# Kernel tuning notes

Measured on AMD Instinct MI355X. Metric: run time of the kernel, lower is better.

The kernel has to match this reference:

```python
import jax, jax.numpy as jnp
import numpy as np

B, C, H, W = 8, 80, 128, 128
K = 100
MAX_OBJS = 128
N_GT = 256  # 32 GT boxes per image
HM_W, WH_W, OFF_W = 1.0, 0.1, 1.0
BETA = 0.1  # iou_map weight ('Ct IoU Loss x 0.1')


def setup_inputs() -> dict:
    key = jax.random.key(0)
    ks = jax.random.split(key, 12)
    hm = jax.random.normal(ks[0], (B, C, H, W), jnp.float32)
    wh = jax.random.normal(ks[1], (B, 2, H, W), jnp.float32) * 2.0 + 8.0
    reg = jax.random.normal(ks[2], (B, 2, H, W), jnp.float32) * 0.1
    hm_target = jax.random.uniform(ks[3], (B, C, H, W), jnp.float32) * 0.99
    wh_target = jax.random.uniform(ks[4], (B, MAX_OBJS, 2), jnp.float32) * 20.0 + 2.0
    reg_target = jax.random.uniform(ks[5], (B, MAX_OBJS, 2), jnp.float32)
    reg_mask = jax.random.randint(ks[6], (B, MAX_OBJS), 0, 2).astype(jnp.int32)
    ind = jax.random.randint(ks[7], (B, MAX_OBJS), 0, H * W).astype(jnp.int32)
    cx = jax.random.uniform(ks[8], (N_GT,)) * (W - 1)
    cy = jax.random.uniform(ks[9], (N_GT,)) * (H - 1)
    bw = jax.random.uniform(ks[10], (N_GT,)) * 30.0 + 2.0
    bh = jax.random.uniform(ks[11], (N_GT,)) * 30.0 + 2.0
    target_box = jnp.stack([cx - bw / 2, cy - bh / 2, cx + bw / 2, cy + bh / 2], -1).astype(jnp.float32)
    target_bidx = jnp.repeat(jnp.arange(B), N_GT // B).astype(jnp.int32)
    return {"hm": hm, "wh": wh, "reg": reg, "hm_target": hm_target,
            "wh_target": wh_target, "reg_target": reg_target,
            "reg_mask": reg_mask, "ind": ind,
            "target_box": target_box, "target_bidx": target_bidx}


def _gather_feat(feat, ind):
    # feat [B, ch, H, W], ind [B, M] spatial indices -> [B, M, ch]
    b, ch = feat.shape[0], feat.shape[1]
    f = feat.reshape(b, ch, -1).transpose(0, 2, 1)  # [B, HW, ch]
    return jnp.take_along_axis(f, ind[:, :, None], axis=1)


def _pairwise_iou(boxes1, boxes2):
    # boxes1 [K,4], boxes2 [N,4], xyxy -> [K,N]
    a1 = jnp.maximum(boxes1[:, 2] - boxes1[:, 0], 0.0) * jnp.maximum(boxes1[:, 3] - boxes1[:, 1], 0.0)
    a2 = jnp.maximum(boxes2[:, 2] - boxes2[:, 0], 0.0) * jnp.maximum(boxes2[:, 3] - boxes2[:, 1], 0.0)
    lt = jnp.maximum(boxes1[:, None, :2], boxes2[None, :, :2])
    rb = jnp.minimum(boxes1[:, None, 2:], boxes2[None, :, 2:])
    whi = jnp.clip(rb - lt, 0.0)
    inter = whi[..., 0] * whi[..., 1]
    union = a1[:, None] + a2[None, :] - inter
    return inter / jnp.maximum(union, 1e-7)


def _decode(hm_s, wh, reg):
    # _nms: 3x3 max-pool peak keeping
    hmax = jax.lax.reduce_window(hm_s, -jnp.inf, jax.lax.max,
                                 (1, 1, 3, 3), (1, 1, 1, 1),
                                 [(0, 0), (0, 0), (1, 1), (1, 1)])
    hm_k = jnp.where(hmax == hm_s, hm_s, 0.0)
    # global top-K over C*H*W (equivalent to per-class topK then topK-of-topK)
    scores, inds = jax.lax.top_k(hm_k.reshape(B, -1), K)
    clses = inds // (H * W)
    sinds = inds % (H * W)
    ys_i = sinds // W
    xs_i = sinds % W
    r = _gather_feat(reg, sinds)  # [B,K,2] sub-pixel offsets
    xs = xs_i.astype(jnp.float32) + r[..., 0]
    ys = ys_i.astype(jnp.float32) + r[..., 1]
    w = _gather_feat(wh, sinds)   # [B,K,2]
    boxes = jnp.stack([xs - w[..., 0] / 2, ys - w[..., 1] / 2,
                       xs + w[..., 0] / 2, ys + w[..., 1] / 2], -1)
    return boxes, scores, clses, ys_i, xs_i


def _focal_loss(pred, gt):
    # CenterNet focal loss; pred already sigmoid+clamped
    pos = gt == 1.0
    neg_w = (1.0 - gt) ** 4
    pos_loss = jnp.sum(jnp.where(pos, jnp.log(pred) * (1.0 - pred) ** 2, 0.0))
    neg_loss = jnp.sum(jnp.where(pos, 0.0, jnp.log(1.0 - pred) * pred ** 2 * neg_w))
    num_pos = jnp.sum(pos.astype(jnp.float32))
    return jnp.where(num_pos > 0, -(pos_loss + neg_loss) / jnp.maximum(num_pos, 1.0), -neg_loss)


def _reg_l1(out, mask, ind, tgt):
    pred = _gather_feat(out, ind)                       # [B, M, 2]
    m = jnp.broadcast_to(mask.astype(jnp.float32)[:, :, None], pred.shape)
    return jnp.sum(jnp.abs(pred * m - tgt * m)) / (jnp.sum(m) + 1e-4)


def reference(hm, wh, reg, hm_target, wh_target, reg_target, reg_mask, ind, target_box, target_bidx):
    hm_s = jnp.clip(jax.nn.sigmoid(hm), 1e-4, 1.0 - 1e-4)  # _sigmoid
    boxes, scores, clses, ys_i, xs_i = _decode(hm_s, wh, reg)
    # per-image pairwise IoU vs GT boxes of the same image, max over GT
    iou_all = jax.vmap(lambda bx: _pairwise_iou(bx, target_box))(boxes)  # [B,K,N]
    bmask = target_bidx[None, None, :] == jnp.arange(B)[:, None, None]
    iou = jnp.max(jnp.where(bmask, iou_all, 0.0), axis=-1)              # [B,K]
    # scatter IoU into dense heatmap-shaped iou_map at (b, cls, y, x)
    b_idx = jnp.broadcast_to(jnp.arange(B)[:, None], (B, K))
    iou_map = jnp.zeros_like(hm_s).at[b_idx, clses, ys_i, xs_i].set(iou)
    hm_t = jnp.clip(hm_target + BETA * iou_map, 0.0, 1.0)
    hm_loss = _focal_loss(hm_s, hm_t)
    wh_loss = _reg_l1(wh, reg_mask, ind, wh_target)
    off_loss = _reg_l1(reg, reg_mask, ind, reg_target)
    loss = HM_W * hm_loss + WH_W * wh_loss + OFF_W * off_loss
    return loss, hm_loss, wh_loss, off_loss
```

## Files before the change

### kernel.cpp

```cpp
#include <hip/hip_runtime.h>
#include <math.h>

#define B_ 8
#define C_ 80
#define H_ 128
#define W_ 128
#define K_ 100
#define MAXOBJS_ 128
#define NGT_ 256
#define HW_ (H_*W_)
#define CHW_ (C_*H_*W_)
#define TOT_ (B_*CHW_)
#define NBINS_ 4096
#define BCAP_ 4096
#define DCAP_ 128
#define CAPLDS_ 1536
#define DLOC_ 128
#define BLOC_ 768
#define NEGINF_ (-INFINITY)

#define OFF_LISTCNT 96
#define OFF_HIST   128
#define OFF_THR    131200
#define OFF_CNTA   131264
#define OFF_CNTB   131296
#define OFF_DEFV   131328
#define OFF_DEFI   135424
#define OFF_BORV   139520
#define OFF_BORI   270592
#define OFF_LIST   401664
#define ZERO_BYTES 131328
#define CAP_REQ    196608ull
#define CAP_MAX    262144ull

__device__ __forceinline__ unsigned skey(float x){
    unsigned u = __float_as_uint(x);
    return (u & 0x80000000u) ? ~u : (u | 0x80000000u);
}

__device__ __forceinline__ void find_thr(const unsigned* __restrict__ lh,
                                         unsigned* __restrict__ part,
                                         unsigned target,
                                         unsigned* out_thr, unsigned* out_cum){
    int t = threadIdx.x;
    unsigned s = 0;
    #pragma unroll
    for(int k=0;k<16;++k) s += lh[t*16+k];
    part[t] = s;
    __syncthreads();
    for(int off=1; off<256; off<<=1){
        unsigned v = (t+off<256) ? part[t+off] : 0u;
        __syncthreads();
        part[t] += v;
        __syncthreads();
    }
    unsigned nxt = (t<255) ? part[t+1] : 0u;
    if(part[t] >= target && nxt < target){
        unsigned cum = nxt;
        int thr = t*16;
        for(int bin=t*16+15; bin>=t*16; --bin){
            unsigned c = lh[bin];
            if(cum + c >= target){ thr = bin; break; }
            cum += c;
        }
        *out_thr = (unsigned)thr;
        *out_cum = cum;
    }
    __syncthreads();
}

struct Row { float v[4]; float le, re; };

__device__ __forceinline__ Row loadrow(const float* __restrict__ P, int y, int xq){
    Row r;
    if(y < 0 || y >= H_){
        r.v[0]=r.v[1]=r.v[2]=r.v[3]=r.le=r.re=NEGINF_;
        return r;
    }
    const float4 f = *(const float4*)(P + y*W_ + xq*4);
    r.v[0]=f.x; r.v[1]=f.y; r.v[2]=f.z; r.v[3]=f.w;
    r.le = (xq==0) ? NEGINF_ : P[y*W_ + xq*4 - 1];
    r.re = (xq==31)? NEGINF_ : P[y*W_ + xq*4 + 4];
    return r;
}

__device__ __forceinline__ void hmax4(const Row& r, float h[4]){
    h[0]=fmaxf(fmaxf(r.le,  r.v[0]), r.v[1]);
    h[1]=fmaxf(fmaxf(r.v[0],r.v[1]), r.v[2]);
    h[2]=fmaxf(fmaxf(r.v[1],r.v[2]), r.v[3]);
    h[3]=fmaxf(fmaxf(r.v[2],r.v[3]), r.re);
}

__global__ __launch_bounds__(256) void k_main(const float* __restrict__ hm,
        const float* __restrict__ hmt, unsigned* __restrict__ hist,
        double* __restrict__ accum, unsigned* __restrict__ listcnt,
        int2* __restrict__ list, int capB){
    __shared__ unsigned lh[NBINS_];
    __shared__ int2 lbuf[CAPLDS_];
    __shared__ unsigned lcnt, lbase;
    __shared__ float red[256];
    int t = threadIdx.x;
    int plane = blockIdx.x >> 1;
    int half  = blockIdx.x & 1;
    int b = plane / C_;
    int cls = plane - b*C_;
    const float* P = hm  + (size_t)plane*HW_;
    const float* T = hmt + (size_t)plane*HW_;
    int idx0 = cls*HW_;
    unsigned lane = (unsigned)(t & 63);

    for(int i=t;i<NBINS_;i+=256) lh[i]=0u;
    if(t==0) lcnt=0u;
    __syncthreads();

    int xq = t & 31;
    int y0 = half*64 + (t >> 5) * 8;
    Row rp = loadrow(P, y0-1, xq);
    Row rc = loadrow(P, y0,   xq);
    float hp[4], hc[4];
    hmax4(rp, hp); hmax4(rc, hc);
    float acc = 0.f;
    for(int rr=0; rr<8; ++rr){
        int y = y0 + rr;
        Row rn = loadrow(P, y+1, xq);
        float hn[4]; hmax4(rn, hn);
        float lr[4];
        lr[0]=fmaxf(rc.le,  rc.v[1]);
        lr[1]=fmaxf(rc.v[0],rc.v[2]);
        lr[2]=fmaxf(rc.v[1],rc.v[3]);
        lr[3]=fmaxf(rc.v[2],rc.re);
        float4 tg = *(const float4*)(T + y*W_ + xq*4);
        float tgv[4] = {tg.x, tg.y, tg.z, tg.w};
        #pragma unroll
        for(int j=0;j<4;++j){
            float v = rc.v[j];
            bool pk = (v>=lr[j]) && (v>=hp[j]) && (v>=hn[j]);
            if(pk) atomicAdd(&lh[skey(v)>>20], 1u);
            if(capB){
                unsigned long long mask = __ballot(pk);
                int cnt = __popcll(mask);
                unsigned pre = (unsigned)__popcll(mask & ((1ull<<lane)-1ull));
                int base = 0;
                if(cnt){
                    if(lane==0) base = (int)atomicAdd(&lcnt, (unsigned)cnt);
                    base = __shfl(base, 0, 64);
                }
                if(pk){
                    unsigned p = (unsigned)base + pre;
                    int2 e; e.x = __float_as_int(v); e.y = idx0 + y*W_ + xq*4 + j;
                    if(p < CAPLDS_) lbuf[p] = e;
                    else {
                        unsigned g = atomicAdd(&listcnt[b], 1u);
                        if(g < (unsigned)capB) list[(size_t)b*capB + g] = e;
                    }
                }
            }
            float pr = 1.f/(1.f + __expf(-v));
            pr = fminf(fmaxf(pr, 1e-4f), 1.f - 1e-4f);
            float q = 1.f - tgv[j]; float q2 = q*q;
            acc += __logf(1.f - pr) * pr * pr * q2 * q2;
        }
        rc = rn;
        #pragma unroll
        for(int j=0;j<4;++j){ hp[j]=hc[j]; hc[j]=hn[j]; }
    }
    __syncthreads();
    unsigned n = lcnt; if(n > CAPLDS_) n = CAPLDS_;
    if(capB && t==0) lbase = atomicAdd(&listcnt[b], n);
    for(int i=t;i<NBINS_;i+=256){ unsigned c=lh[i]; if(c) atomicAdd(&hist[b*NBINS_+i], c); }
    red[t] = acc;
    __syncthreads();
    if(capB){
        for(unsigned i=t;i<n;i+=256){
            unsigned g = lbase + i;
            if(g < (unsigned)capB) list[(size_t)b*capB + g] = lbuf[i];
        }
    }
    for(int s=128;s>0;s>>=1){
        if(t<s) red[t]+=red[t+s];
        __syncthreads();
    }
    if(t==0) atomicAdd(&accum[0], (double)red[0]);
}

__global__ void k_thresh(const unsigned* __restrict__ hist, unsigned* __restrict__ thrbin){
    __shared__ unsigned lh[NBINS_];
    __shared__ unsigned part[256];
    __shared__ unsigned thrs, cums;
    int b = blockIdx.x, t = threadIdx.x;
    for(int i=t;i<NBINS_;i+=256) lh[i]=hist[b*NBINS_+i];
    if(t==0){ thrs=0u; cums=0u; }
    __syncthreads();
    find_thr(lh, part, (unsigned)K_, &thrs, &cums);
    if(t==0) thrbin[b]=thrs;
}

__global__ __launch_bounds__(256) void k_scan(const int2* __restrict__ list,
        const unsigned* __restrict__ listcnt, int capB,
        const unsigned* __restrict__ thrbin,
        unsigned* __restrict__ cntA, unsigned* __restrict__ cntB,
        float* __restrict__ defv, int* __restrict__ defi,
        float* __restrict__ borv, int* __restrict__ bori){
    __shared__ int2 dloc[DLOC_];
    __shared__ int2 bloc[BLOC_];
    __shared__ unsigned dc, bc, dbase, bbase;
    int b = blockIdx.x >> 6;
    int chunk = blockIdx.x & 63;
    int t = threadIdx.x;
    if(t==0){ dc=0u; bc=0u; }
    __syncthreads();
    unsigned thr = thrbin[b];
    unsigned n = listcnt[b]; if(n > (unsigned)capB) n = (unsigned)capB;
    for(unsigned i = chunk*256u + t; i < n; i += 64u*256u){
        int2 e = list[(size_t)b*capB + i];
        float v = __int_as_float(e.x);
        unsigned bin = skey(v) >> 20;
        if(bin > thr){
            unsigned p = atomicAdd(&dc, 1u);
            if(p < DLOC_) dloc[p] = e;
            else { unsigned g = atomicAdd(&cntA[b],1u); if(g<DCAP_){ defv[b*DCAP_+g]=v; defi[b*DCAP_+g]=e.y; } }
        } else if(bin == thr){
            unsigned p = atomicAdd(&bc, 1u);
            if(p < BLOC_) bloc[p] = e;
            else { unsigned g = atomicAdd(&cntB[b],1u); if(g<BCAP_){ borv[b*BCAP_+g]=v; bori[b*BCAP_+g]=e.y; } }
        }
    }
    __syncthreads();
    unsigned dn = dc < DLOC_ ? dc : DLOC_;
    unsigned bn = bc < BLOC_ ? bc : BLOC_;
    if(t==0){
        dbase = dn ? atomicAdd(&cntA[b], dn) : 0u;
        bbase = bn ? atomicAdd(&cntB[b], bn) : 0u;
    }
    __syncthreads();
    for(unsigned i=t;i<dn;i+=256){
        unsigned g = dbase + i;
        if(g < DCAP_){ defv[b*DCAP_+g]=__int_as_float(dloc[i].x); defi[b*DCAP_+g]=dloc[i].y; }
    }
    for(unsigned i=t;i<bn;i+=256){
        unsigned g = bbase + i;
        if(g < BCAP_){ borv[b*BCAP_+g]=__int_as_float(bloc[i].x); bori[b*BCAP_+g]=bloc[i].y; }
    }
}

__device__ __forceinline__ bool is_peak_scalar(const float* __restrict__ hm, int idx, float v){
    int w = idx & (W_-1);
    int h = (idx >> 7) & (H_-1);
    bool peak = true;
    #pragma unroll
    for(int dy=-1; dy<=1; ++dy){
        int hh = h + dy;
        if(hh < 0 || hh >= H_) continue;
        #pragma unroll
        for(int dx=-1; dx<=1; ++dx){
            if(dy==0 && dx==0) continue;
            int ww = w + dx;
            if(ww < 0 || ww >= W_) continue;
            peak = peak && (v >= __ldg(&hm[idx + dy*W_ + dx]));
        }
    }
    return peak;
}

__global__ __launch_bounds__(256) void k_collect(const float* __restrict__ hm,
        const unsigned* __restrict__ thrbin,
        unsigned* __restrict__ cntA, unsigned* __restrict__ cntB,
        float* __restrict__ defv, int* __restrict__ defi,
        float* __restrict__ borv, int* __restrict__ bori){
    int idx = blockIdx.x*256 + threadIdx.x;
    float v = hm[idx];
    if(!is_peak_scalar(hm, idx, v)) return;
    int b = idx / CHW_;
    unsigned bin = skey(v) >> 20;
    unsigned thr = thrbin[b];
    if(bin > thr){
        unsigned p = atomicAdd(&cntA[b], 1u);
        if(p < DCAP_){ defv[b*DCAP_+p] = v; defi[b*DCAP_+p] = idx - b*CHW_; }
    } else if(bin == thr){
        unsigned p = atomicAdd(&cntB[b], 1u);
        if(p < BCAP_){ borv[b*BCAP_+p] = v; bori[b*BCAP_+p] = idx - b*CHW_; }
    }
}

__global__ __launch_bounds__(256) void k_select(const float* __restrict__ hm,
        const float* __restrict__ hmt, const float* __restrict__ wh,
        const float* __restrict__ reg, const float* __restrict__ tbox,
        const int* __restrict__ tbid,
        const unsigned* __restrict__ cntA, const unsigned* __restrict__ cntB,
        const float* __restrict__ defv, const int* __restrict__ defi,
        const float* __restrict__ borv, const int* __restrict__ bori,
        double* __restrict__ accum, int* __restrict__ misc){
    int b = blockIdx.x, t = threadIdx.x;
    __shared__ float sbox[NGT_][4];
    __shared__ int   sbid[NGT_];
    __shared__ float sv[BCAP_];
    __shared__ int   si[BCAP_];
    __shared__ unsigned h2[NBINS_];
    __shared__ unsigned t4[BCAP_];
    __shared__ unsigned part[256];
    __shared__ int  rvI[256];
    __shared__ int  sel[K_];
    __shared__ unsigned selc, t3c, t4c;
    __shared__ unsigned thr2s, cum2s, thr3s, need3s;
    __shared__ int wsel;

    int nA = (int)cntA[b]; if(nA>DCAP_) nA=DCAP_; if(nA>K_) nA=K_;
    int nB = (int)cntB[b]; if(nB>BCAP_) nB=BCAP_;
    int m = K_ - nA; if(m>nB) m=nB; if(m<0) m=0;

    for(int i=t;i<NGT_;i+=256){
        sbox[i][0]=tbox[i*4+0]; sbox[i][1]=tbox[i*4+1];
        sbox[i][2]=tbox[i*4+2]; sbox[i][3]=tbox[i*4+3];
        sbid[i]=tbid[i];
    }
    for(int i=t;i<nB;i+=256){ sv[i]=borv[b*BCAP_+i]; si[i]=bori[b*BCAP_+i]; }
    for(int i=t;i<nA;i+=256) sel[i]=defi[b*DCAP_+i];
    if(t==0){ selc=(unsigned)nA; t3c=0u; t4c=0u; thr2s=0u; cum2s=0u; thr3s=0u; need3s=0u; }
    for(int i=t;i<NBINS_;i+=256) h2[i]=0u;
    __syncthreads();

    if(m>0){
        for(int i=t;i<nB;i+=256) atomicAdd(&h2[(skey(sv[i])>>8)&0xFFFu], 1u);
        __syncthreads();
        find_thr(h2, part, (unsigned)m, &thr2s, &cum2s);
        unsigned thr2 = thr2s, need2 = (unsigned)m - cum2s;
        for(int i=t;i<nB;i+=256){
            unsigned sb=(skey(sv[i])>>8)&0xFFFu;
            if(sb>thr2){ unsigned p=atomicAdd(&selc,1u); if(p<K_) sel[p]=si[i]; }
            else if(sb==thr2){ unsigned p=atomicAdd(&t3c,1u); if(p<BCAP_) t4[p]=(unsigned)i; }
        }
        __syncthreads();
        unsigned nt3=t3c; if(nt3>BCAP_) nt3=BCAP_;
        part[t]=0u;
        __syncthreads();
        for(unsigned i=t;i<nt3;i+=256) atomicAdd(&part[skey(sv[t4[i]])&0xFFu], 1u);
        __syncthreads();
        for(int off=1; off<256; off<<=1){
            unsigned v = (t+off<256)? part[t+off] : 0u;
            __syncthreads();
            part[t] += v;
            __syncthreads();
        }
        {
            unsigned nxt = (t<255)? part[t+1] : 0u;
            if(part[t] >= need2 && nxt < need2){ thr3s=(unsigned)t; need3s=need2-nxt; }
        }
        __syncthreads();
        unsigned thr3=thr3s, need3=need3s;
        for(unsigned i=t;i<nt3;i+=256){
            unsigned ci=t4[i];
            unsigned lb=skey(sv[ci])&0xFFu;
            if(lb>thr3){ unsigned p=atomicAdd(&selc,1u); if(p<K_) sel[p]=si[ci]; }
            else if(lb==thr3){ unsigned p=atomicAdd(&t4c,1u); if(p<NBINS_) h2[p]=(unsigned)si[ci]; }
        }
        __syncthreads();
        unsigned n4=t4c; if(n4>NBINS_) n4=NBINS_;
        if(need3 >= n4){
            for(unsigned i=t;i<n4;i+=256){ unsigned p=atomicAdd(&selc,1u); if(p<K_) sel[p]=(int)h2[i]; }
            __syncthreads();
        } else {
            for(unsigned it=0; it<need3; ++it){
                int bi=0x7FFFFFFF;
                for(unsigned i=t;i<n4;i+=256){ int w=(int)h2[i]; bi = (w<bi)?w:bi; }
                rvI[t]=bi;
                __syncthreads();
                for(int st=128;st>0;st>>=1){
                    if(t<st){ int w=rvI[t+st]; if(w<rvI[t]) rvI[t]=w; }
                    __syncthreads();
                }
                if(t==0){ wsel=rvI[0]; unsigned p=selc; selc=p+1u; if(p<K_) sel[p]=wsel; }
                __syncthreads();
                int w=wsel;
                for(unsigned i=t;i<n4;i+=256) if((int)h2[i]==w) h2[i]=0x7FFFFFFFu;
                __syncthreads();
            }
        }
    }
    __syncthreads();

    int nsel=(int)selc; if(nsel>K_) nsel=K_;
    for(int k=t;k<nsel;k+=256){
        int idx = sel[k];
        int cls = idx / HW_;
        int sp  = idx - cls*HW_;
        int yi  = sp >> 7;
        int xi  = sp & (W_-1);
        float r0 = reg[(b*2+0)*HW_ + sp];
        float r1 = reg[(b*2+1)*HW_ + sp];
        float w0 = wh[(b*2+0)*HW_ + sp];
        float w1 = wh[(b*2+1)*HW_ + sp];
        float xs = (float)xi + r0;
        float ys = (float)yi + r1;
        float x1 = xs - w0*0.5f, y1 = ys - w1*0.5f;
        float x2 = xs + w0*0.5f, y2 = ys + w1*0.5f;
        float a1 = fmaxf(x2-x1, 0.f) * fmaxf(y2-y1, 0.f);
        float best = 0.f;
        for(int g=0; g<NGT_; ++g){
            if(sbid[g] != b) continue;
            float gx1=sbox[g][0], gy1=sbox[g][1], gx2=sbox[g][2], gy2=sbox[g][3];
            float a2 = fmaxf(gx2-gx1, 0.f) * fmaxf(gy2-gy1, 0.f);
            float ix1 = fmaxf(x1,gx1), iy1 = fmaxf(y1,gy1);
            float ix2 = fminf(x2,gx2), iy2 = fminf(y2,gy2);
            float iw = fmaxf(ix2-ix1, 0.f), ih = fmaxf(iy2-iy1, 0.f);
            float inter = iw*ih;
            float uni = a1 + a2 - inter;
            float iou = inter / fmaxf(uni, 1e-7f);
            best = fmaxf(best, iou);
        }
        int gidx = b*CHW_ + idx;
        float v = hm[gidx];
        float p = 1.f/(1.f + __expf(-v));
        p = fminf(fmaxf(p, 1e-4f), 1.f - 1e-4f);
        float gt0 = hmt[gidx];
        float q0 = 1.f - gt0; float q02 = q0*q0;
        float neg0 = __logf(1.f - p) * p * p * q02 * q02;
        float gt1 = fminf(gt0 + 0.1f*best, 1.f);
        if(gt1 == 1.f){
            atomicAdd(&misc[0], 1);
            float op = 1.f - p;
            atomicAdd(&accum[1], (double)(__logf(p)*op*op));
            atomicAdd(&accum[2], (double)(-neg0));
        } else {
            float q1 = 1.f - gt1; float q12 = q1*q1;
            float neg1 = __logf(1.f - p) * p * p * q12 * q12;
            atomicAdd(&accum[2], (double)(neg1 - neg0));
        }
    }
}

__global__ void k_regfinal(const float* __restrict__ wh, const float* __restrict__ reg,
        const float* __restrict__ wht, const float* __restrict__ regt,
        const int* __restrict__ mask, const int* __restrict__ ind,
        const double* __restrict__ accum, const int* __restrict__ misc,
        float* __restrict__ out){
    int tid = threadIdx.x;
    float whn = 0.f, offn = 0.f, ms = 0.f;
    for(int i=tid; i<B_*MAXOBJS_; i+=256){
        int b = i / MAXOBJS_;
        float mk = (float)mask[i];
        int id = ind[i];
        float p0 = wh[(b*2+0)*HW_ + id], p1 = wh[(b*2+1)*HW_ + id];
        whn += mk*(fabsf(p0 - wht[2*i]) + fabsf(p1 - wht[2*i+1]));
        float q0 = reg[(b*2+0)*HW_ + id], q1 = reg[(b*2+1)*HW_ + id];
        offn += mk*(fabsf(q0 - regt[2*i]) + fabsf(q1 - regt[2*i+1]));
        ms += 2.f*mk;
    }
    __shared__ float r0[256], r1[256], r2[256];
    r0[tid]=whn; r1[tid]=offn; r2[tid]=ms;
    __syncthreads();
    for(int st=128; st>0; st>>=1){
        if(tid<st){ r0[tid]+=r0[tid+st]; r1[tid]+=r1[tid+st]; r2[tid]+=r2[tid+st]; }
        __syncthreads();
    }
    if(tid==0){
        double neg = accum[0] + accum[2];
        double pos = accum[1];
        int np = misc[0];
        float hm_loss;
        if(np > 0) hm_loss = (float)(-(pos + neg) / (double)(np < 1 ? 1 : np));
        else       hm_loss = (float)(-neg);
        float msum = r2[0];
        float wh_loss  = r0[0] / (msum + 1e-4f);
        float off_loss = r1[0] / (msum + 1e-4f);
        float loss = hm_loss + 0.1f*wh_loss + off_loss;
        out[0]=loss; out[1]=hm_loss; out[2]=wh_loss; out[3]=off_loss;
    }
}

extern "C" void kernel_launch(void* const* d_in, const int* in_sizes, int n_in,
                              void* d_out, int out_size, void* d_ws, size_t ws_size,
                              hipStream_t stream){
    const float* hm   = (const float*)d_in[0];
    const float* wh   = (const float*)d_in[1];
    const float* reg  = (const float*)d_in[2];
    const float* hmt  = (const float*)d_in[3];
    const float* wht  = (const float*)d_in[4];
    const float* regt = (const float*)d_in[5];
    const int*   mask = (const int*)d_in[6];
    const int*   ind  = (const int*)d_in[7];
    const float* tbox = (const float*)d_in[8];
    const int*   tbid = (const int*)d_in[9];

    char* ws = (char*)d_ws;
    double*   accum   = (double*)ws;
    int*      misc    = (int*)(ws + 64);
    unsigned* listcnt = (unsigned*)(ws + OFF_LISTCNT);
    unsigned* hist    = (unsigned*)(ws + OFF_HIST);
    unsigned* thrbin  = (unsigned*)(ws + OFF_THR);
    unsigned* cntA    = (unsigned*)(ws + OFF_CNTA);
    unsigned* cntB    = (unsigned*)(ws + OFF_CNTB);
    float*    defv    = (float*)(ws + OFF_DEFV);
    int*      defi    = (int*)(ws + OFF_DEFI);
    float*    borv    = (float*)(ws + OFF_BORV);
    int*      bori    = (int*)(ws + OFF_BORI);
    int2*     list    = (int2*)(ws + OFF_LIST);

    size_t capB = 0;
    if(ws_size >= (size_t)OFF_LIST + CAP_REQ*(size_t)B_*8ull){
        capB = (ws_size - (size_t)OFF_LIST) / ((size_t)B_*8ull);
        if(capB > CAP_MAX) capB = CAP_MAX;
    }

    hipMemsetAsync(ws, 0, ZERO_BYTES, stream);
    k_main<<<B_*C_*2, 256, 0, stream>>>(hm, hmt, hist, accum, listcnt, list, (int)capB);
    k_thresh<<<B_, 256, 0, stream>>>(hist, thrbin);
    if(capB){
        k_scan<<<B_*64, 256, 0, stream>>>(list, listcnt, (int)capB, thrbin,
                                          cntA, cntB, defv, defi, borv, bori);
    } else {
        k_collect<<<TOT_/256, 256, 0, stream>>>(hm, thrbin, cntA, cntB,
                                                defv, defi, borv, bori);
    }
    k_select<<<B_, 256, 0, stream>>>(hm, hmt, wh, reg, tbox, tbid, cntA, cntB,
                                     defv, defi, borv, bori, accum, misc);
    k_regfinal<<<1, 256, 0, stream>>>(wh, reg, wht, regt, mask, ind, accum, misc,
                                      (float*)d_out);
    (void)in_sizes; (void)n_in; (void)out_size;
}
```

Measured before the change: 98.93 us.

## Fuse threshold and final reduction into preceding kernels via last-block counters

```diff
diff --git a/kernel.cpp b/kernel.cpp
--- a/kernel.cpp
+++ b/kernel.cpp
@@ -14,24 +14,27 @@
 #define NBINS_ 4096
 #define BCAP_ 4096
 #define DCAP_ 128
-#define CAPLDS_ 1536
+#define CAPLDS_ 1024
 #define DLOC_ 128
 #define BLOC_ 768
 #define NEGINF_ (-INFINITY)
 
+#define OFF_MISC    64
 #define OFF_LISTCNT 96
-#define OFF_HIST   128
-#define OFF_THR    131200
-#define OFF_CNTA   131264
-#define OFF_CNTB   131296
-#define OFF_DEFV   131328
-#define OFF_DEFI   135424
-#define OFF_BORV   139520
-#define OFF_BORI   270592
-#define OFF_LIST   401664
-#define ZERO_BYTES 131328
-#define CAP_REQ    196608ull
-#define CAP_MAX    262144ull
+#define OFF_BDONE   128
+#define OFF_SELDONE 160
+#define OFF_THRB    192
+#define OFF_CNTA    224
+#define OFF_CNTB    256
+#define OFF_HIST    512
+#define ZERO_BYTES  131584
+#define OFF_DEFV    131584
+#define OFF_DEFI    135680
+#define OFF_BORV    139776
+#define OFF_BORI    270848
+#define OFF_LIST    401920
+#define CAP_REQ     196608ull
+#define CAP_MAX     262144ull
 
 __device__ __forceinline__ unsigned skey(float x){
     unsigned u = __float_as_uint(x);
@@ -69,36 +72,69 @@
     __syncthreads();
 }
 
-struct Row { float v[4]; float le, re; };
-
-__device__ __forceinline__ Row loadrow(const float* __restrict__ P, int y, int xq){
-    Row r;
-    if(y < 0 || y >= H_){
-        r.v[0]=r.v[1]=r.v[2]=r.v[3]=r.le=r.re=NEGINF_;
-        return r;
-    }
-    const float4 f = *(const float4*)(P + y*W_ + xq*4);
-    r.v[0]=f.x; r.v[1]=f.y; r.v[2]=f.z; r.v[3]=f.w;
-    r.le = (xq==0) ? NEGINF_ : P[y*W_ + xq*4 - 1];
-    r.re = (xq==31)? NEGINF_ : P[y*W_ + xq*4 + 4];
-    return r;
-}
-
-__device__ __forceinline__ void hmax4(const Row& r, float h[4]){
-    h[0]=fmaxf(fmaxf(r.le,  r.v[0]), r.v[1]);
-    h[1]=fmaxf(fmaxf(r.v[0],r.v[1]), r.v[2]);
-    h[2]=fmaxf(fmaxf(r.v[1],r.v[2]), r.v[3]);
-    h[3]=fmaxf(fmaxf(r.v[2],r.v[3]), r.re);
+__device__ __forceinline__ void find_thr_g(const unsigned* __restrict__ gh,
+                                           unsigned* __restrict__ part,
+                                           unsigned target,
+                                           unsigned* out_thr, unsigned* out_cum){
+    int t = threadIdx.x;
+    unsigned loc[16]; unsigned s = 0;
+    #pragma unroll
+    for(int k=0;k<16;++k){
+        loc[k] = __hip_atomic_load(&gh[t*16+k], __ATOMIC_RELAXED, __HIP_MEMORY_SCOPE_AGENT);
+        s += loc[k];
+    }
+    part[t] = s;
+    __syncthreads();
+    for(int off=1; off<256; off<<=1){
+        unsigned v = (t+off<256) ? part[t+off] : 0u;
+        __syncthreads();
+        part[t] += v;
+        __syncthreads();
+    }
+    unsigned nxt = (t<255) ? part[t+1] : 0u;
+    if(part[t] >= target && nxt < target){
+        unsigned cum = nxt; int thr = t*16; bool fnd = false;
+        #pragma unroll
+        for(int k=15;k>=0;--k){
+            if(!fnd){
+                if(cum + loc[k] >= target){ thr = t*16+k; fnd = true; }
+                else cum += loc[k];
+            }
+        }
+        *out_thr = (unsigned)thr;
+        *out_cum = cum;
+    }
+    __syncthreads();
+}
+
+__device__ __forceinline__ void loadrow(const float* __restrict__ P, int y, int xq,
+                                        float4& f, float& le, float& re){
+    if(y >= 0 && y < H_) f = *(const float4*)(P + y*W_ + xq*4);
+    else { f.x = NEGINF_; f.y = NEGINF_; f.z = NEGINF_; f.w = NEGINF_; }
+    float l = __shfl_up(f.w, 1, 32);
+    float r = __shfl_down(f.x, 1, 32);
+    le = (xq==0)  ? NEGINF_ : l;
+    re = (xq==31) ? NEGINF_ : r;
+}
+
+__device__ __forceinline__ void hmax4v(const float4& f, float le, float re, float h[4]){
+    h[0]=fmaxf(fmaxf(le,  f.x), f.y);
+    h[1]=fmaxf(fmaxf(f.x, f.y), f.z);
+    h[2]=fmaxf(fmaxf(f.y, f.z), f.w);
+    h[3]=fmaxf(fmaxf(f.z, f.w), re);
 }
 
 __global__ __launch_bounds__(256) void k_main(const float* __restrict__ hm,
         const float* __restrict__ hmt, unsigned* __restrict__ hist,
         double* __restrict__ accum, unsigned* __restrict__ listcnt,
-        int2* __restrict__ list, int capB){
-    __shared__ unsigned lh[NBINS_];
+        int2* __restrict__ list, int capB, unsigned* __restrict__ bdone,
+        unsigned* __restrict__ thrbin){
+    __shared__ unsigned lhp[NBINS_/2];
     __shared__ int2 lbuf[CAPLDS_];
-    __shared__ unsigned lcnt, lbase;
-    __shared__ float red[256];
+    __shared__ unsigned part[256];
+    __shared__ float wsum[4];
+    __shared__ unsigned lcnt, lbase, thrs, cums;
+    __shared__ int amlast;
     int t = threadIdx.x;
     int plane = blockIdx.x >> 1;
     int half  = blockIdx.x & 1;
@@ -107,46 +143,43 @@
     const float* P = hm  + (size_t)plane*HW_;
     const float* T = hmt + (size_t)plane*HW_;
     int idx0 = cls*HW_;
-    unsigned lane = (unsigned)(t & 63);
-
-    for(int i=t;i<NBINS_;i+=256) lh[i]=0u;
-    if(t==0) lcnt=0u;
+
+    for(int i=t;i<NBINS_/2;i+=256) lhp[i]=0u;
+    if(t==0){ lcnt=0u; thrs=0u; cums=0u; }
     __syncthreads();
 
     int xq = t & 31;
-    int y0 = half*64 + (t >> 5) * 8;
-    Row rp = loadrow(P, y0-1, xq);
-    Row rc = loadrow(P, y0,   xq);
-    float hp[4], hc[4];
-    hmax4(rp, hp); hmax4(rc, hc);
+    int y0 = half*64 + (t>>5)*8;
+
+    float4 vp; float lep, rep;
+    loadrow(P, y0-1, xq, vp, lep, rep);
+    float hp[4]; hmax4v(vp, lep, rep, hp);
+    float4 vc; float lec, rec;
+    loadrow(P, y0, xq, vc, lec, rec);
+
     float acc = 0.f;
     for(int rr=0; rr<8; ++rr){
         int y = y0 + rr;
-        Row rn = loadrow(P, y+1, xq);
-        float hn[4]; hmax4(rn, hn);
-        float lr[4];
-        lr[0]=fmaxf(rc.le,  rc.v[1]);
-        lr[1]=fmaxf(rc.v[0],rc.v[2]);
-        lr[2]=fmaxf(rc.v[1],rc.v[3]);
-        lr[3]=fmaxf(rc.v[2],rc.re);
+        float4 vn; float len, ren;
+        loadrow(P, y+1, xq, vn, len, ren);
+        float hn[4]; hmax4v(vn, len, ren, hn);
+        float vv[4]  = {vc.x, vc.y, vc.z, vc.w};
+        float lrv[4];
+        lrv[0]=fmaxf(lec,  vc.y);
+        lrv[1]=fmaxf(vc.x, vc.z);
+        lrv[2]=fmaxf(vc.y, vc.w);
+        lrv[3]=fmaxf(vc.z, rec);
         float4 tg = *(const float4*)(T + y*W_ + xq*4);
         float tgv[4] = {tg.x, tg.y, tg.z, tg.w};
         #pragma unroll
         for(int j=0;j<4;++j){
-            float v = rc.v[j];
-            bool pk = (v>=lr[j]) && (v>=hp[j]) && (v>=hn[j]);
-            if(pk) atomicAdd(&lh[skey(v)>>20], 1u);
-            if(capB){
-                unsigned long long mask = __ballot(pk);
-                int cnt = __popcll(mask);
-                unsigned pre = (unsigned)__popcll(mask & ((1ull<<lane)-1ull));
-                int base = 0;
-                if(cnt){
-                    if(lane==0) base = (int)atomicAdd(&lcnt, (unsigned)cnt);
-                    base = __shfl(base, 0, 64);
-                }
-                if(pk){
-                    unsigned p = (unsigned)base + pre;
+            float v = vv[j];
+            bool pk = (v>=lrv[j]) && (v>=hp[j]) && (v>=hn[j]);
+            if(pk){
+                unsigned bin = skey(v)>>20;
+                atomicAdd(&lhp[bin>>1], 1u<<((bin&1)<<4));
+                if(capB){
+                    unsigned p = atomicAdd(&lcnt, 1u);
                     int2 e; e.x = __float_as_int(v); e.y = idx0 + y*W_ + xq*4 + j;
                     if(p < CAPLDS_) lbuf[p] = e;
                     else {
@@ -160,15 +193,25 @@
             float q = 1.f - tgv[j]; float q2 = q*q;
             acc += __logf(1.f - pr) * pr * pr * q2 * q2;
         }
-        rc = rn;
         #pragma unroll
-        for(int j=0;j<4;++j){ hp[j]=hc[j]; hc[j]=hn[j]; }
-    }
-    __syncthreads();
+        for(int j=0;j<4;++j) hp[j] = fmaxf(lrv[j], vv[j]);
+        vc = vn; lec = len; rec = ren;
+    }
+    __syncthreads();
+
     unsigned n = lcnt; if(n > CAPLDS_) n = CAPLDS_;
     if(capB && t==0) lbase = atomicAdd(&listcnt[b], n);
-    for(int i=t;i<NBINS_;i+=256){ unsigned c=lh[i]; if(c) atomicAdd(&hist[b*NBINS_+i], c); }
-    red[t] = acc;
+    for(int i=t;i<NBINS_/2;i+=256){
+        unsigned w = lhp[i];
+        if(w){
+            unsigned c0 = w & 0xFFFFu, c1 = w >> 16;
+            if(c0) atomicAdd(&hist[b*NBINS_ + 2*i],     c0);
+            if(c1) atomicAdd(&hist[b*NBINS_ + 2*i + 1], c1);
+        }
+    }
+    #pragma unroll
+    for(int off=32; off>0; off>>=1) acc += __shfl_xor(acc, off, 64);
+    if((t & 63) == 0) wsum[t>>6] = acc;
     __syncthreads();
     if(capB){
         for(unsigned i=t;i<n;i+=256){
@@ -176,23 +219,20 @@
             if(g < (unsigned)capB) list[(size_t)b*capB + g] = lbuf[i];
         }
     }
-    for(int s=128;s>0;s>>=1){
-        if(t<s) red[t]+=red[t+s];
-        __syncthreads();
-    }
-    if(t==0) atomicAdd(&accum[0], (double)red[0]);
-}
-
-__global__ void k_thresh(const unsigned* __restrict__ hist, unsigned* __restrict__ thrbin){
-    __shared__ unsigned lh[NBINS_];
-    __shared__ unsigned part[256];
-    __shared__ unsigned thrs, cums;
-    int b = blockIdx.x, t = threadIdx.x;
-    for(int i=t;i<NBINS_;i+=256) lh[i]=hist[b*NBINS_+i];
-    if(t==0){ thrs=0u; cums=0u; }
-    __syncthreads();
-    find_thr(lh, part, (unsigned)K_, &thrs, &cums);
-    if(t==0) thrbin[b]=thrs;
+    if(t==0) atomicAdd(&accum[0], (double)(wsum[0]+wsum[1]+wsum[2]+wsum[3]));
+
+    __threadfence();
+    __syncthreads();
+    if(t==0){
+        unsigned d = atomicAdd(&bdone[b], 1u);
+        amlast = (d == (unsigned)(2*C_ - 1));
+    }
+    __syncthreads();
+    if(amlast){
+        __threadfence();
+        find_thr_g(&hist[b*NBINS_], part, (unsigned)K_, &thrs, &cums);
+        if(t==0) thrbin[b] = thrs;
+    }
 }
 
 __global__ __launch_bounds__(256) void k_scan(const int2* __restrict__ list,
@@ -286,13 +326,16 @@
         const float* __restrict__ hmt, const float* __restrict__ wh,
         const float* __restrict__ reg, const float* __restrict__ tbox,
         const int* __restrict__ tbid,
+        const float* __restrict__ wht, const float* __restrict__ regt,
+        const int* __restrict__ mask, const int* __restrict__ ind,
         const unsigned* __restrict__ cntA, const unsigned* __restrict__ cntB,
         const float* __restrict__ defv, const int* __restrict__ defi,
         const float* __restrict__ borv, const int* __restrict__ bori,
-        double* __restrict__ accum, int* __restrict__ misc){
+        double* __restrict__ accum, int* __restrict__ misc,
+        unsigned* __restrict__ seldone, float* __restrict__ out){
     int b = blockIdx.x, t = threadIdx.x;
-    __shared__ float sbox[NGT_][4];
-    __shared__ int   sbid[NGT_];
+    __shared__ float gbox[NGT_][4];
+    __shared__ float garea[NGT_];
     __shared__ float sv[BCAP_];
     __shared__ int   si[BCAP_];
     __shared__ unsigned h2[NBINS_];
@@ -300,23 +343,33 @@
     __shared__ unsigned part[256];
     __shared__ int  rvI[256];
     __shared__ int  sel[K_];
-    __shared__ unsigned selc, t3c, t4c;
+    __shared__ float sbx[K_][4];
+    __shared__ float sa[K_];
+    __shared__ int   ioui[K_];
+    __shared__ float r0s[256], r1s[256], r2s[256];
+    __shared__ unsigned gcnt, selc, t3c, t4c;
     __shared__ unsigned thr2s, cum2s, thr3s, need3s;
-    __shared__ int wsel;
+    __shared__ int wsel, amlast;
 
     int nA = (int)cntA[b]; if(nA>DCAP_) nA=DCAP_; if(nA>K_) nA=K_;
     int nB = (int)cntB[b]; if(nB>BCAP_) nB=BCAP_;
     int m = K_ - nA; if(m>nB) m=nB; if(m<0) m=0;
 
+    if(t==0){ gcnt=0u; selc=(unsigned)nA; t3c=0u; t4c=0u;
+              thr2s=0u; cum2s=0u; thr3s=0u; need3s=0u; }
+    for(int i=t;i<NBINS_;i+=256) h2[i]=0u;
+    __syncthreads();
+
     for(int i=t;i<NGT_;i+=256){
-        sbox[i][0]=tbox[i*4+0]; sbox[i][1]=tbox[i*4+1];
-        sbox[i][2]=tbox[i*4+2]; sbox[i][3]=tbox[i*4+3];
-        sbid[i]=tbid[i];
+        if(tbid[i]==b){
+            unsigned p = atomicAdd(&gcnt, 1u);
+            float gx1=tbox[i*4+0], gy1=tbox[i*4+1], gx2=tbox[i*4+2], gy2=tbox[i*4+3];
+            gbox[p][0]=gx1; gbox[p][1]=gy1; gbox[p][2]=gx2; gbox[p][3]=gy2;
+            garea[p]=fmaxf(gx2-gx1,0.f)*fmaxf(gy2-gy1,0.f);
+        }
     }
     for(int i=t;i<nB;i+=256){ sv[i]=borv[b*BCAP_+i]; si[i]=bori[b*BCAP_+i]; }
     for(int i=t;i<nA;i+=256) sel[i]=defi[b*DCAP_+i];
-    if(t==0){ selc=(unsigned)nA; t3c=0u; t4c=0u; thr2s=0u; cum2s=0u; thr3s=0u; need3s=0u; }
-    for(int i=t;i<NBINS_;i+=256) h2[i]=0u;
     __syncthreads();
 
     if(m>0){
@@ -383,31 +436,32 @@
         int idx = sel[k];
         int cls = idx / HW_;
         int sp  = idx - cls*HW_;
-        int yi  = sp >> 7;
-        int xi  = sp & (W_-1);
-        float r0 = reg[(b*2+0)*HW_ + sp];
-        float r1 = reg[(b*2+1)*HW_ + sp];
-        float w0 = wh[(b*2+0)*HW_ + sp];
-        float w1 = wh[(b*2+1)*HW_ + sp];
-        float xs = (float)xi + r0;
-        float ys = (float)yi + r1;
-        float x1 = xs - w0*0.5f, y1 = ys - w1*0.5f;
-        float x2 = xs + w0*0.5f, y2 = ys + w1*0.5f;
-        float a1 = fmaxf(x2-x1, 0.f) * fmaxf(y2-y1, 0.f);
-        float best = 0.f;
-        for(int g=0; g<NGT_; ++g){
-            if(sbid[g] != b) continue;
-            float gx1=sbox[g][0], gy1=sbox[g][1], gx2=sbox[g][2], gy2=sbox[g][3];
-            float a2 = fmaxf(gx2-gx1, 0.f) * fmaxf(gy2-gy1, 0.f);
-            float ix1 = fmaxf(x1,gx1), iy1 = fmaxf(y1,gy1);
-            float ix2 = fminf(x2,gx2), iy2 = fminf(y2,gy2);
-            float iw = fmaxf(ix2-ix1, 0.f), ih = fmaxf(iy2-iy1, 0.f);
-            float inter = iw*ih;
-            float uni = a1 + a2 - inter;
-            float iou = inter / fmaxf(uni, 1e-7f);
-            best = fmaxf(best, iou);
-        }
-        int gidx = b*CHW_ + idx;
+        int yi = sp>>7, xi = sp&(W_-1);
+        float rr0 = reg[(b*2+0)*HW_+sp], rr1 = reg[(b*2+1)*HW_+sp];
+        float w0 = wh[(b*2+0)*HW_+sp],  w1 = wh[(b*2+1)*HW_+sp];
+        float xs = (float)xi + rr0, ys = (float)yi + rr1;
+        float x1=xs-w0*0.5f, y1=ys-w1*0.5f, x2=xs+w0*0.5f, y2=ys+w1*0.5f;
+        sbx[k][0]=x1; sbx[k][1]=y1; sbx[k][2]=x2; sbx[k][3]=y2;
+        sa[k] = fmaxf(x2-x1,0.f)*fmaxf(y2-y1,0.f);
+        ioui[k] = 0;
+    }
+    __syncthreads();
+    int ng = (int)gcnt; if(ng>NGT_) ng=NGT_;
+    for(int pi=t; pi<nsel*ng; pi+=256){
+        int k = pi / ng, g = pi - k*ng;
+        float x1=sbx[k][0], y1=sbx[k][1], x2=sbx[k][2], y2=sbx[k][3];
+        float ix1=fmaxf(x1,gbox[g][0]), iy1=fmaxf(y1,gbox[g][1]);
+        float ix2=fminf(x2,gbox[g][2]), iy2=fminf(y2,gbox[g][3]);
+        float iw=fmaxf(ix2-ix1,0.f), ih=fmaxf(iy2-iy1,0.f);
+        float inter=iw*ih;
+        float uni = sa[k] + garea[g] - inter;
+        float iou = inter / fmaxf(uni, 1e-7f);
+        atomicMax(&ioui[k], __float_as_int(iou));
+    }
+    __syncthreads();
+    for(int k=t;k<nsel;k+=256){
+        float best = __int_as_float(ioui[k]);
+        int gidx = b*CHW_ + sel[k];
         float v = hm[gidx];
         float p = 1.f/(1.f + __expf(-v));
         p = fminf(fmaxf(p, 1e-4f), 1.f - 1e-4f);
@@ -426,44 +480,46 @@
             atomicAdd(&accum[2], (double)(neg1 - neg0));
         }
     }
-}
-
-__global__ void k_regfinal(const float* __restrict__ wh, const float* __restrict__ reg,
-        const float* __restrict__ wht, const float* __restrict__ regt,
-        const int* __restrict__ mask, const int* __restrict__ ind,
-        const double* __restrict__ accum, const int* __restrict__ misc,
-        float* __restrict__ out){
-    int tid = threadIdx.x;
-    float whn = 0.f, offn = 0.f, ms = 0.f;
-    for(int i=tid; i<B_*MAXOBJS_; i+=256){
-        int b = i / MAXOBJS_;
-        float mk = (float)mask[i];
-        int id = ind[i];
-        float p0 = wh[(b*2+0)*HW_ + id], p1 = wh[(b*2+1)*HW_ + id];
-        whn += mk*(fabsf(p0 - wht[2*i]) + fabsf(p1 - wht[2*i+1]));
-        float q0 = reg[(b*2+0)*HW_ + id], q1 = reg[(b*2+1)*HW_ + id];
-        offn += mk*(fabsf(q0 - regt[2*i]) + fabsf(q1 - regt[2*i+1]));
-        ms += 2.f*mk;
-    }
-    __shared__ float r0[256], r1[256], r2[256];
-    r0[tid]=whn; r1[tid]=offn; r2[tid]=ms;
-    __syncthreads();
-    for(int st=128; st>0; st>>=1){
-        if(tid<st){ r0[tid]+=r0[tid+st]; r1[tid]+=r1[tid+st]; r2[tid]+=r2[tid+st]; }
-        __syncthreads();
-    }
-    if(tid==0){
-        double neg = accum[0] + accum[2];
-        double pos = accum[1];
-        int np = misc[0];
-        float hm_loss;
-        if(np > 0) hm_loss = (float)(-(pos + neg) / (double)(np < 1 ? 1 : np));
-        else       hm_loss = (float)(-neg);
-        float msum = r2[0];
-        float wh_loss  = r0[0] / (msum + 1e-4f);
-        float off_loss = r1[0] / (msum + 1e-4f);
-        float loss = hm_loss + 0.1f*wh_loss + off_loss;
-        out[0]=loss; out[1]=hm_loss; out[2]=wh_loss; out[3]=off_loss;
+
+    __threadfence();
+    __syncthreads();
+    if(t==0){
+        unsigned d = atomicAdd(seldone, 1u);
+        amlast = (d == (unsigned)(B_-1));
+    }
+    __syncthreads();
+    if(amlast){
+        __threadfence();
+        float whn=0.f, offn=0.f, ms=0.f;
+        for(int i=t;i<B_*MAXOBJS_;i+=256){
+            int bb = i >> 7;
+            float mk = (float)mask[i];
+            int id = ind[i];
+            float p0 = wh[(bb*2+0)*HW_+id], p1 = wh[(bb*2+1)*HW_+id];
+            whn += mk*(fabsf(p0 - wht[2*i]) + fabsf(p1 - wht[2*i+1]));
+            float q0 = reg[(bb*2+0)*HW_+id], q1 = reg[(bb*2+1)*HW_+id];
+            offn += mk*(fabsf(q0 - regt[2*i]) + fabsf(q1 - regt[2*i+1]));
+            ms += 2.f*mk;
+        }
+        r0s[t]=whn; r1s[t]=offn; r2s[t]=ms;
+        __syncthreads();
+        for(int st=128; st>0; st>>=1){
+            if(t<st){ r0s[t]+=r0s[t+st]; r1s[t]+=r1s[t+st]; r2s[t]+=r2s[t+st]; }
+            __syncthreads();
+        }
+        if(t==0){
+            double nb  = __hip_atomic_load(&accum[0], __ATOMIC_RELAXED, __HIP_MEMORY_SCOPE_AGENT);
+            double pos = __hip_atomic_load(&accum[1], __ATOMIC_RELAXED, __HIP_MEMORY_SCOPE_AGENT);
+            double nd  = __hip_atomic_load(&accum[2], __ATOMIC_RELAXED, __HIP_MEMORY_SCOPE_AGENT);
+            int np = __hip_atomic_load(&misc[0], __ATOMIC_RELAXED, __HIP_MEMORY_SCOPE_AGENT);
+            double neg = nb + nd;
+            float hm_loss = (np > 0) ? (float)(-(pos + neg)/(double)np) : (float)(-neg);
+            float msum = r2s[0];
+            float wh_loss  = r0s[0] / (msum + 1e-4f);
+            float off_loss = r1s[0] / (msum + 1e-4f);
+            out[0] = hm_loss + 0.1f*wh_loss + off_loss;
+            out[1] = hm_loss; out[2] = wh_loss; out[3] = off_loss;
+        }
     }
 }
 
@@ -483,12 +539,14 @@
 
     char* ws = (char*)d_ws;
     double*   accum   = (double*)ws;
-    int*      misc    = (int*)(ws + 64);
+    int*      misc    = (int*)(ws + OFF_MISC);
     unsigned* listcnt = (unsigned*)(ws + OFF_LISTCNT);
-    unsigned* hist    = (unsigned*)(ws + OFF_HIST);
-    unsigned* thrbin  = (unsigned*)(ws + OFF_THR);
+    unsigned* bdone   = (unsigned*)(ws + OFF_BDONE);
+    unsigned* seldone = (unsigned*)(ws + OFF_SELDONE);
+    unsigned* thrbin  = (unsigned*)(ws + OFF_THRB);
     unsigned* cntA    = (unsigned*)(ws + OFF_CNTA);
     unsigned* cntB    = (unsigned*)(ws + OFF_CNTB);
+    unsigned* hist    = (unsigned*)(ws + OFF_HIST);
     float*    defv    = (float*)(ws + OFF_DEFV);
     int*      defi    = (int*)(ws + OFF_DEFI);
     float*    borv    = (float*)(ws + OFF_BORV);
@@ -502,8 +560,8 @@
     }
 
     hipMemsetAsync(ws, 0, ZERO_BYTES, stream);
-    k_main<<<B_*C_*2, 256, 0, stream>>>(hm, hmt, hist, accum, listcnt, list, (int)capB);
-    k_thresh<<<B_, 256, 0, stream>>>(hist, thrbin);
+    k_main<<<B_*C_*2, 256, 0, stream>>>(hm, hmt, hist, accum, listcnt, list,
+                                        (int)capB, bdone, thrbin);
     if(capB){
         k_scan<<<B_*64, 256, 0, stream>>>(list, listcnt, (int)capB, thrbin,
                                           cntA, cntB, defv, defi, borv, bori);
@@ -511,9 +569,9 @@
         k_collect<<<TOT_/256, 256, 0, stream>>>(hm, thrbin, cntA, cntB,
                                                 defv, defi, borv, bori);
     }
-    k_select<<<B_, 256, 0, stream>>>(hm, hmt, wh, reg, tbox, tbid, cntA, cntB,
-                                     defv, defi, borv, bori, accum, misc);
-    k_regfinal<<<1, 256, 0, stream>>>(wh, reg, wht, regt, mask, ind, accum, misc,
-                                      (float*)d_out);
+    k_select<<<B_, 256, 0, stream>>>(hm, hmt, wh, reg, tbox, tbid,
+                                     wht, regt, mask, ind, cntA, cntB,
+                                     defv, defi, borv, bori, accum, misc,
+                                     seldone, (float*)d_out);
     (void)in_sizes; (void)n_in; (void)out_size;
 }
```

Result: slower. 208.3 us (+110.5%).
